# Kernel optimization log

Measured on AMD Instinct MI355X. Metric: run time of the kernel, lower is better.

The kernel has to match this reference:

```python
import jax, jax.numpy as jnp
import numpy as np

B, N, E, C, H = 2, 50000, 800000, 128, 512  # batch, nodes, edges, feat, 4*feat


def setup_inputs() -> dict:
    key = jax.random.key(0)
    ks = jax.random.split(key, 11)
    s_in = 1.0 / np.sqrt(C)
    s_h = 1.0 / np.sqrt(H)
    return {
        "graph_sig": jax.random.normal(ks[0], (B, N, C), dtype=jnp.float32),
        "edge_index": jax.random.randint(ks[1], (2, E), 0, N, dtype=jnp.int64),
        "W1_0": jax.random.normal(ks[2], (C, H), dtype=jnp.float32) * s_in,
        "b1_0": jnp.zeros((H,), dtype=jnp.float32),
        "W2_0": jax.random.normal(ks[3], (H, C), dtype=jnp.float32) * s_h,
        "b2_0": jnp.zeros((C,), dtype=jnp.float32),
        "W1_1": jax.random.normal(ks[4], (C, H), dtype=jnp.float32) * s_in,
        "b1_1": jnp.zeros((H,), dtype=jnp.float32),
        "W2_1": jax.random.normal(ks[5], (H, C), dtype=jnp.float32) * s_h,
        "b2_1": jnp.zeros((C,), dtype=jnp.float32),
    }


def gin_layer(x, src, dst, W1, b1, W2, b2):
    # GINConv with eps=0: h_i = MLP((1+eps)*x_i + sum_{j->i} x_j)
    # gather source features along edges, scatter-add into destinations
    agg = jnp.zeros_like(x).at[:, dst, :].add(x[:, src, :])  # (B, N, C)
    h = agg + x
    h = jax.nn.relu(jnp.einsum('bnc,ch->bnh', h, W1) + b1)
    return jnp.einsum('bnh,hc->bnc', h, W2) + b2


def reference(graph_sig, edge_index, W1_0, b1_0, W2_0, b2_0, W1_1, b1_1, W2_1, b2_1):
    src, dst = edge_index[0], edge_index[1]
    x = gin_layer(graph_sig, src, dst, W1_0, b1_0, W2_0, b2_0)
    x = gin_layer(x, src, dst, W1_1, b1_1, W2_1, b2_1)
    return x
```

## Files before the change

kernel.cpp:

```cpp
#include <hip/hip_runtime.h>

#define CDIM 128
#define HDIM 512
#define NB 2
#define NNODES 50000
#define NEDGES 800000
#define ROWS (NB * NNODES)

typedef _Float16 half8 __attribute__((ext_vector_type(8)));
typedef _Float16 half4 __attribute__((ext_vector_type(4)));
typedef float f32x4 __attribute__((ext_vector_type(4)));

__device__ __forceinline__ f32x4 mfma_f16(half8 a, half8 b, f32x4 c) {
  return __builtin_amdgcn_mfma_f32_16x16x32_f16(a, b, c, 0, 0, 0);
}

#define GLOAD_LDS16(g, l)                                                      \
  __builtin_amdgcn_global_load_lds(                                            \
      (const __attribute__((address_space(1))) void*)(g),                      \
      (__attribute__((address_space(3))) void*)(l), 16, 0, 0)

__global__ void hist_k(const int* __restrict__ ei, int* __restrict__ counts) {
  int e = blockIdx.x * 256 + threadIdx.x;
  if (e < NEDGES) atomicAdd(&counts[ei[NEDGES + e]], 1);
}

#define SC_BLOCKS 13

__global__ __launch_bounds__(256) void scan1_k(const int* __restrict__ counts,
                                               int* __restrict__ bsum) {
  __shared__ int ws[4];
  int i0 = blockIdx.x * 4096 + threadIdx.x * 16;
  int s = 0;
#pragma unroll
  for (int k = 0; k < 16; ++k) {
    int i = i0 + k;
    s += (i < NNODES) ? counts[i] : 0;
  }
#pragma unroll
  for (int off = 1; off < 64; off <<= 1) s += __shfl_down(s, off);
  if ((threadIdx.x & 63) == 0) ws[threadIdx.x >> 6] = s;
  __syncthreads();
  if (threadIdx.x == 0) bsum[blockIdx.x] = ws[0] + ws[1] + ws[2] + ws[3];
}

__global__ void scan2_k(const int* __restrict__ bsum, int* __restrict__ bbase,
                        int* __restrict__ offsets) {
  int run = 0;
  for (int b = 0; b < SC_BLOCKS; ++b) {
    bbase[b] = run;
    run += bsum[b];
  }
  offsets[NNODES] = run;
}

__global__ __launch_bounds__(256) void scan3_k(const int* __restrict__ counts,
                                               const int* __restrict__ bbase,
                                               int* __restrict__ offsets,
                                               int* __restrict__ cursor) {
  __shared__ int sm[256];
  int i0 = blockIdx.x * 4096 + threadIdx.x * 16;
  int v[16];
  int tsum = 0;
#pragma unroll
  for (int k = 0; k < 16; ++k) {
    int i = i0 + k;
    v[k] = (i < NNODES) ? counts[i] : 0;
    tsum += v[k];
  }
  sm[threadIdx.x] = tsum;
  __syncthreads();
  for (int off = 1; off < 256; off <<= 1) {
    int t = (threadIdx.x >= off) ? sm[threadIdx.x - off] : 0;
    __syncthreads();
    sm[threadIdx.x] += t;
    __syncthreads();
  }
  int run = bbase[blockIdx.x] + sm[threadIdx.x] - tsum;
#pragma unroll
  for (int k = 0; k < 16; ++k) {
    int i = i0 + k;
    if (i < NNODES) {
      offsets[i] = run;
      cursor[i] = run;
    }
    run += v[k];
  }
}

__global__ void fill_k(const int* __restrict__ ei, int* __restrict__ cursor,
                       int* __restrict__ col) {
  int e = blockIdx.x * 256 + threadIdx.x;
  if (e < NEDGES) {
    int d = ei[NEDGES + e];
    int p = atomicAdd(&cursor[d], 1);
    col[p] = ei[e];
  }
}

__global__ void cvt16i_k(const float* __restrict__ s, _Float16* __restrict__ d) {
  const int PB = NNODES * CDIM;
  int i = blockIdx.x * 256 + threadIdx.x;
  int str = gridDim.x * 256;
  for (; i < ROWS * (CDIM / 8); i += str) {
    size_t flat = (size_t)i * 8;
    int b = (int)(flat / PB);
    size_t r = flat - (size_t)b * PB;
    int n = (int)(r >> 7);
    int c0 = (int)(r & 127);
    float4 f0 = *(const float4*)(s + flat);
    float4 f1 = *(const float4*)(s + flat + 4);
    half8 o;
    o[0] = (_Float16)f0.x; o[1] = (_Float16)f0.y;
    o[2] = (_Float16)f0.z; o[3] = (_Float16)f0.w;
    o[4] = (_Float16)f1.x; o[5] = (_Float16)f1.y;
    o[6] = (_Float16)f1.z; o[7] = (_Float16)f1.w;
    *(half8*)(d + ((size_t)n * 2 + b) * CDIM + c0) = o;
  }
}

__global__ __launch_bounds__(256) void aggi_k(const _Float16* __restrict__ x,
                                              const int* __restrict__ offs,
                                              const int* __restrict__ col,
                                              _Float16* __restrict__ h) {
  int node = blockIdx.x * 4 + (threadIdx.x >> 6);
  int lane = threadIdx.x & 63;
  if (node >= NNODES) return;
  const half4* xp = (const half4*)x;
  half4 self = xp[(size_t)node * 64 + lane];
  float a0 = (float)self[0], a1 = (float)self[1], a2 = (float)self[2], a3 = (float)self[3];
  float c0 = 0.f, c1 = 0.f, c2 = 0.f, c3 = 0.f;
  int e = offs[node], e1 = offs[node + 1];
  for (; e + 7 < e1; e += 8) {
    int s0 = col[e], s1 = col[e + 1], s2 = col[e + 2], s3 = col[e + 3];
    int s4 = col[e + 4], s5 = col[e + 5], s6 = col[e + 6], s7 = col[e + 7];
    half4 v0 = xp[(size_t)s0 * 64 + lane];
    half4 v1 = xp[(size_t)s1 * 64 + lane];
    half4 v2 = xp[(size_t)s2 * 64 + lane];
    half4 v3 = xp[(size_t)s3 * 64 + lane];
    half4 v4 = xp[(size_t)s4 * 64 + lane];
    half4 v5 = xp[(size_t)s5 * 64 + lane];
    half4 v6 = xp[(size_t)s6 * 64 + lane];
    half4 v7 = xp[(size_t)s7 * 64 + lane];
    a0 += (float)v0[0] + (float)v1[0] + (float)v2[0] + (float)v3[0];
    a1 += (float)v0[1] + (float)v1[1] + (float)v2[1] + (float)v3[1];
    a2 += (float)v0[2] + (float)v1[2] + (float)v2[2] + (float)v3[2];
    a3 += (float)v0[3] + (float)v1[3] + (float)v2[3] + (float)v3[3];
    c0 += (float)v4[0] + (float)v5[0] + (float)v6[0] + (float)v7[0];
    c1 += (float)v4[1] + (float)v5[1] + (float)v6[1] + (float)v7[1];
    c2 += (float)v4[2] + (float)v5[2] + (float)v6[2] + (float)v7[2];
    c3 += (float)v4[3] + (float)v5[3] + (float)v6[3] + (float)v7[3];
  }
  for (; e + 1 < e1; e += 2) {
    int s0 = col[e], s1 = col[e + 1];
    half4 v0 = xp[(size_t)s0 * 64 + lane];
    half4 v1 = xp[(size_t)s1 * 64 + lane];
    a0 += (float)v0[0]; a1 += (float)v0[1];
    a2 += (float)v0[2]; a3 += (float)v0[3];
    c0 += (float)v1[0]; c1 += (float)v1[1];
    c2 += (float)v1[2]; c3 += (float)v1[3];
  }
  if (e < e1) {
    int s0 = col[e];
    half4 v0 = xp[(size_t)s0 * 64 + lane];
    a0 += (float)v0[0]; a1 += (float)v0[1];
    a2 += (float)v0[2]; a3 += (float)v0[3];
  }
  half4 r;
  r[0] = (_Float16)(a0 + c0);
  r[1] = (_Float16)(a1 + c1);
  r[2] = (_Float16)(a2 + c2);
  r[3] = (_Float16)(a3 + c3);
  ((half4*)h)[(size_t)node * 64 + lane] = r;
}

__global__ void pack_mlp(const float* __restrict__ W1, const float* __restrict__ W2,
                         _Float16* __restrict__ dst) {
  int tid = blockIdx.x * 256 + threadIdx.x;
  if (tid >= 16384) return;
  int l = tid & 63;
  int g = (tid >> 6) & 7;
  int c = (tid >> 9) & 15;
  int isW2 = tid >> 13;
  int lg = l >> 4, l15 = l & 15;
  _Float16* o;
  if (!isW2) {
    int jt = g >> 2, ks = g & 3;
    int k0 = ks * 32 + lg * 8;
    int n = c * 32 + jt * 16 + l15;
    o = dst + (size_t)c * 8192 + g * 512 + l * 8;
#pragma unroll
    for (int i = 0; i < 8; ++i) o[i] = (_Float16)W1[(size_t)(k0 + i) * HDIM + n];
  } else {
    int k0 = c * 32 + lg * 8;
    int n = g * 16 + l15;
    o = dst + (size_t)c * 8192 + 4096 + g * 512 + l * 8;
#pragma unroll
    for (int i = 0; i < 8; ++i) o[i] = (_Float16)W2[(size_t)(k0 + i) * CDIM + n];
  }
}

template <typename OT, bool REMAP>
__global__ __launch_bounds__(256, 4) void mlp_v3(
    const _Float16* __restrict__ hin, const _Float16* __restrict__ wpk,
    const float* __restrict__ b1, const float* __restrict__ b2,
    OT* __restrict__ out) {
  __shared__ alignas(16) _Float16 wbuf[2][8192];
  __shared__ alignas(16) _Float16 tbuf[4][32 * 32];

  const int tidx = threadIdx.x;
  const int lane = tidx & 63;
  const int wid = tidx >> 6;
  const int l15 = lane & 15, lg = lane >> 4;
  const long long r0 = (long long)blockIdx.x * 128 + wid * 32;

  half8 A[2][4];
#pragma unroll
  for (int rt = 0; rt < 2; ++rt) {
    long long row = r0 + rt * 16 + l15;
    if (row >= ROWS) row = ROWS - 1;
    const _Float16* hp = hin + row * CDIM + lg * 8;
#pragma unroll
    for (int ks = 0; ks < 4; ++ks) A[rt][ks] = *(const half8*)(hp + ks * 32);
  }

  {
    const _Float16* src = wpk;
#pragma unroll
    for (int q = 0; q < 4; ++q) {
      int s = wid * 4 + q;
      GLOAD_LDS16(src + s * 512 + lane * 8, &wbuf[0][s * 512]);
    }
  }
  __syncthreads();

  f32x4 acc[2][8];
#pragma unroll
  for (int rt = 0; rt < 2; ++rt)
#pragma unroll
    for (int ct = 0; ct < 8; ++ct) acc[rt][ct] = (f32x4){0.f, 0.f, 0.f, 0.f};

  _Float16* tw = &tbuf[wid][0];

  for (int c = 0; c < 16; ++c) {
    const int cur = c & 1;
    if (c + 1 < 16) {
      const _Float16* src = wpk + (size_t)(c + 1) * 8192;
#pragma unroll
      for (int q = 0; q < 4; ++q) {
        int s = wid * 4 + q;
        GLOAD_LDS16(src + s * 512 + lane * 8, &wbuf[cur ^ 1][s * 512]);
      }
    }
    const _Float16* w1c = &wbuf[cur][0];
    const _Float16* w2c = &wbuf[cur][4096];

#pragma unroll
    for (int jt = 0; jt < 2; ++jt) {
      f32x4 t0 = (f32x4){0.f, 0.f, 0.f, 0.f};
      f32x4 t1 = (f32x4){0.f, 0.f, 0.f, 0.f};
#pragma unroll
      for (int ks = 0; ks < 4; ++ks) {
        half8 b = *(const half8*)(w1c + (jt * 4 + ks) * 512 + lane * 8);
        t0 = mfma_f16(A[0][ks], b, t0);
        t1 = mfma_f16(A[1][ks], b, t1);
      }
      float bb = b1[c * 32 + jt * 16 + l15];
      int j = jt * 16 + l15;
#pragma unroll
      for (int r = 0; r < 4; ++r) {
        int n0 = lg * 4 + r;
        tw[n0 * 32 + (j ^ (((n0 >> 2) & 3) << 3))] = (_Float16)fmaxf(t0[r] + bb, 0.f);
        int n1 = 16 + lg * 4 + r;
        tw[n1 * 32 + (j ^ (((n1 >> 2) & 3) << 3))] = (_Float16)fmaxf(t1[r] + bb, 0.f);
      }
    }

    half8 ta0, ta1;
    {
      int n = l15;
      ta0 = *(const half8*)(tw + n * 32 + ((lg * 8) ^ (((n >> 2) & 3) << 3)));
      n = 16 + l15;
      ta1 = *(const half8*)(tw + n * 32 + ((lg * 8) ^ (((n >> 2) & 3) << 3)));
    }
#pragma unroll
    for (int ct = 0; ct < 8; ++ct) {
      half8 b = *(const half8*)(w2c + ct * 512 + lane * 8);
      acc[0][ct] = mfma_f16(ta0, b, acc[0][ct]);
      acc[1][ct] = mfma_f16(ta1, b, acc[1][ct]);
    }
    __syncthreads();
  }

#pragma unroll
  for (int ct = 0; ct < 8; ++ct) {
    float b2v = b2[ct * 16 + l15];
#pragma unroll
    for (int rt = 0; rt < 2; ++rt) {
#pragma unroll
      for (int r = 0; r < 4; ++r) {
        long long g = r0 + rt * 16 + lg * 4 + r;
        if (g < ROWS) {
          size_t off;
          if (REMAP) {
            off = (size_t)(g & 1) * NNODES * CDIM + (size_t)(g >> 1) * CDIM + ct * 16 + l15;
          } else {
            off = (size_t)g * CDIM + ct * 16 + l15;
          }
          out[off] = (OT)(acc[rt][ct][r] + b2v);
        }
      }
    }
  }
}

extern "C" void kernel_launch(void* const* d_in, const int* in_sizes, int n_in,
                              void* d_out, int out_size, void* d_ws, size_t ws_size,
                              hipStream_t stream) {
  const float* x0 = (const float*)d_in[0];
  const int* ei = (const int*)d_in[1];
  const float* W1_0 = (const float*)d_in[2];
  const float* b1_0 = (const float*)d_in[3];
  const float* W2_0 = (const float*)d_in[4];
  const float* b2_0 = (const float*)d_in[5];
  const float* W1_1 = (const float*)d_in[6];
  const float* b1_1 = (const float*)d_in[7];
  const float* W2_1 = (const float*)d_in[8];
  const float* b2_1 = (const float*)d_in[9];
  float* out = (float*)d_out;

  _Float16* xh = (_Float16*)d_ws;
  _Float16* hh = xh + (size_t)ROWS * CDIM;
  _Float16* wpk0 = hh + (size_t)ROWS * CDIM;
  _Float16* wpk1 = wpk0 + 131072;
  int* counts = (int*)(wpk1 + 131072);
  int* offsets = counts + NNODES;
  int* cursor = offsets + NNODES + 1;
  int* col = cursor + NNODES;
  int* bsum = col + NEDGES;
  int* bbase = bsum + 16;

  const int eBlocks = (NEDGES + 255) / 256;
  const int aggBlocks = (NNODES + 3) / 4;
  const int mlpBlocks = (ROWS + 127) / 128;

  hipMemsetAsync(counts, 0, NNODES * sizeof(int), stream);
  hist_k<<<eBlocks, 256, 0, stream>>>(ei, counts);
  scan1_k<<<SC_BLOCKS, 256, 0, stream>>>(counts, bsum);
  scan2_k<<<1, 1, 0, stream>>>(bsum, bbase, offsets);
  scan3_k<<<SC_BLOCKS, 256, 0, stream>>>(counts, bbase, offsets, cursor);
  fill_k<<<eBlocks, 256, 0, stream>>>(ei, cursor, col);

  pack_mlp<<<64, 256, 0, stream>>>(W1_0, W2_0, wpk0);
  pack_mlp<<<64, 256, 0, stream>>>(W1_1, W2_1, wpk1);

  cvt16i_k<<<2048, 256, 0, stream>>>(x0, xh);

  aggi_k<<<aggBlocks, 256, 0, stream>>>(xh, offsets, col, hh);
  mlp_v3<_Float16, false><<<mlpBlocks, 256, 0, stream>>>(hh, wpk0, b1_0, b2_0, xh);
  aggi_k<<<aggBlocks, 256, 0, stream>>>(xh, offsets, col, hh);
  mlp_v3<float, true><<<mlpBlocks, 256, 0, stream>>>(hh, wpk1, b1_1, b2_1, out);
}
```

Baseline: 338.4 us.

## Fuse neighbor aggregation into the MLP kernel via shared-memory tile

Merges the CSR gather-sum aggregation and the two-layer MLP into one kernel per GIN layer. Each wave aggregates 16 nodes (32 interleaved batch rows) into an LDS tile, then loads its MFMA A operands from that tile. This removes the global write and re-read of the aggregated features and two kernel launches. In exchange, LDS use per block rises, the launch bound drops from 4 to 2 blocks per SM, and the gather unroll shrinks from 8 to 4, which may reduce memory-level parallelism during the latency-bound gather.

```diff
diff --git a/kernel.cpp b/kernel.cpp
--- a/kernel.cpp
+++ b/kernel.cpp
@@ -119,61 +119,6 @@
   }
 }
 
-__global__ __launch_bounds__(256) void aggi_k(const _Float16* __restrict__ x,
-                                              const int* __restrict__ offs,
-                                              const int* __restrict__ col,
-                                              _Float16* __restrict__ h) {
-  int node = blockIdx.x * 4 + (threadIdx.x >> 6);
-  int lane = threadIdx.x & 63;
-  if (node >= NNODES) return;
-  const half4* xp = (const half4*)x;
-  half4 self = xp[(size_t)node * 64 + lane];
-  float a0 = (float)self[0], a1 = (float)self[1], a2 = (float)self[2], a3 = (float)self[3];
-  float c0 = 0.f, c1 = 0.f, c2 = 0.f, c3 = 0.f;
-  int e = offs[node], e1 = offs[node + 1];
-  for (; e + 7 < e1; e += 8) {
-    int s0 = col[e], s1 = col[e + 1], s2 = col[e + 2], s3 = col[e + 3];
-    int s4 = col[e + 4], s5 = col[e + 5], s6 = col[e + 6], s7 = col[e + 7];
-    half4 v0 = xp[(size_t)s0 * 64 + lane];
-    half4 v1 = xp[(size_t)s1 * 64 + lane];
-    half4 v2 = xp[(size_t)s2 * 64 + lane];
-    half4 v3 = xp[(size_t)s3 * 64 + lane];
-    half4 v4 = xp[(size_t)s4 * 64 + lane];
-    half4 v5 = xp[(size_t)s5 * 64 + lane];
-    half4 v6 = xp[(size_t)s6 * 64 + lane];
-    half4 v7 = xp[(size_t)s7 * 64 + lane];
-    a0 += (float)v0[0] + (float)v1[0] + (float)v2[0] + (float)v3[0];
-    a1 += (float)v0[1] + (float)v1[1] + (float)v2[1] + (float)v3[1];
-    a2 += (float)v0[2] + (float)v1[2] + (float)v2[2] + (float)v3[2];
-    a3 += (float)v0[3] + (float)v1[3] + (float)v2[3] + (float)v3[3];
-    c0 += (float)v4[0] + (float)v5[0] + (float)v6[0] + (float)v7[0];
-    c1 += (float)v4[1] + (float)v5[1] + (float)v6[1] + (float)v7[1];
-    c2 += (float)v4[2] + (float)v5[2] + (float)v6[2] + (float)v7[2];
-    c3 += (float)v4[3] + (float)v5[3] + (float)v6[3] + (float)v7[3];
-  }
-  for (; e + 1 < e1; e += 2) {
-    int s0 = col[e], s1 = col[e + 1];
-    half4 v0 = xp[(size_t)s0 * 64 + lane];
-    half4 v1 = xp[(size_t)s1 * 64 + lane];
-    a0 += (float)v0[0]; a1 += (float)v0[1];
-    a2 += (float)v0[2]; a3 += (float)v0[3];
-    c0 += (float)v1[0]; c1 += (float)v1[1];
-    c2 += (float)v1[2]; c3 += (float)v1[3];
-  }
-  if (e < e1) {
-    int s0 = col[e];
-    half4 v0 = xp[(size_t)s0 * 64 + lane];
-    a0 += (float)v0[0]; a1 += (float)v0[1];
-    a2 += (float)v0[2]; a3 += (float)v0[3];
-  }
-  half4 r;
-  r[0] = (_Float16)(a0 + c0);
-  r[1] = (_Float16)(a1 + c1);
-  r[2] = (_Float16)(a2 + c2);
-  r[3] = (_Float16)(a3 + c3);
-  ((half4*)h)[(size_t)node * 64 + lane] = r;
-}
-
 __global__ void pack_mlp(const float* __restrict__ W1, const float* __restrict__ W2,
                          _Float16* __restrict__ dst) {
   int tid = blockIdx.x * 256 + threadIdx.x;
@@ -201,10 +146,12 @@
 }
 
 template <typename OT, bool REMAP>
-__global__ __launch_bounds__(256, 4) void mlp_v3(
-    const _Float16* __restrict__ hin, const _Float16* __restrict__ wpk,
+__global__ __launch_bounds__(256, 2) void fused_k(
+    const _Float16* __restrict__ x, const int* __restrict__ offs,
+    const int* __restrict__ col, const _Float16* __restrict__ wpk,
     const float* __restrict__ b1, const float* __restrict__ b2,
     OT* __restrict__ out) {
+  __shared__ alignas(16) _Float16 htile[4][16 * 256];
   __shared__ alignas(16) _Float16 wbuf[2][8192];
   __shared__ alignas(16) _Float16 tbuf[4][32 * 32];
 
@@ -213,16 +160,7 @@
   const int wid = tidx >> 6;
   const int l15 = lane & 15, lg = lane >> 4;
   const long long r0 = (long long)blockIdx.x * 128 + wid * 32;
-
-  half8 A[2][4];
-#pragma unroll
-  for (int rt = 0; rt < 2; ++rt) {
-    long long row = r0 + rt * 16 + l15;
-    if (row >= ROWS) row = ROWS - 1;
-    const _Float16* hp = hin + row * CDIM + lg * 8;
-#pragma unroll
-    for (int ks = 0; ks < 4; ++ks) A[rt][ks] = *(const half8*)(hp + ks * 32);
-  }
+  const int nb = blockIdx.x * 64 + wid * 16;
 
   {
     const _Float16* src = wpk;
@@ -232,6 +170,57 @@
       GLOAD_LDS16(src + s * 512 + lane * 8, &wbuf[0][s * 512]);
     }
   }
+
+  const half4* xp = (const half4*)x;
+  _Float16* hw = &htile[wid][0];
+  for (int i = 0; i < 16; ++i) {
+    int node = nb + i;
+    half4 r = (half4){0, 0, 0, 0};
+    if (node < NNODES) {
+      half4 self = xp[(size_t)node * 64 + lane];
+      float a0 = (float)self[0], a1 = (float)self[1];
+      float a2 = (float)self[2], a3 = (float)self[3];
+      float c0 = 0.f, c1 = 0.f, c2 = 0.f, c3 = 0.f;
+      int e = offs[node], e1 = offs[node + 1];
+      for (; e + 3 < e1; e += 4) {
+        int s0 = col[e], s1 = col[e + 1], s2 = col[e + 2], s3 = col[e + 3];
+        half4 v0 = xp[(size_t)s0 * 64 + lane];
+        half4 v1 = xp[(size_t)s1 * 64 + lane];
+        half4 v2 = xp[(size_t)s2 * 64 + lane];
+        half4 v3 = xp[(size_t)s3 * 64 + lane];
+        a0 += (float)v0[0] + (float)v1[0];
+        a1 += (float)v0[1] + (float)v1[1];
+        a2 += (float)v0[2] + (float)v1[2];
+        a3 += (float)v0[3] + (float)v1[3];
+        c0 += (float)v2[0] + (float)v3[0];
+        c1 += (float)v2[1] + (float)v3[1];
+        c2 += (float)v2[2] + (float)v3[2];
+        c3 += (float)v2[3] + (float)v3[3];
+      }
+      for (; e < e1; ++e) {
+        half4 v0 = xp[(size_t)col[e] * 64 + lane];
+        a0 += (float)v0[0];
+        a1 += (float)v0[1];
+        a2 += (float)v0[2];
+        a3 += (float)v0[3];
+      }
+      r[0] = (_Float16)(a0 + c0);
+      r[1] = (_Float16)(a1 + c1);
+      r[2] = (_Float16)(a2 + c2);
+      r[3] = (_Float16)(a3 + c3);
+    }
+    *(half4*)&hw[i * 256 + lane * 4] = r;
+  }
+
+  half8 A[2][4];
+#pragma unroll
+  for (int rt = 0; rt < 2; ++rt) {
+    int rl = rt * 16 + l15;
+    const _Float16* hp = hw + (rl >> 1) * 256 + (rl & 1) * 128 + lg * 8;
+#pragma unroll
+    for (int ks = 0; ks < 4; ++ks) A[rt][ks] = *(const half8*)(hp + ks * 32);
+  }
+
   __syncthreads();
 
   f32x4 acc[2][8];
@@ -341,8 +330,7 @@
   int* bbase = bsum + 16;
 
   const int eBlocks = (NEDGES + 255) / 256;
-  const int aggBlocks = (NNODES + 3) / 4;
-  const int mlpBlocks = (ROWS + 127) / 128;
+  const int fusedBlocks = (NNODES + 63) / 64;
 
   hipMemsetAsync(counts, 0, NNODES * sizeof(int), stream);
   hist_k<<<eBlocks, 256, 0, stream>>>(ei, counts);
@@ -356,8 +344,8 @@
 
   cvt16i_k<<<2048, 256, 0, stream>>>(x0, xh);
 
-  aggi_k<<<aggBlocks, 256, 0, stream>>>(xh, offsets, col, hh);
-  mlp_v3<_Float16, false><<<mlpBlocks, 256, 0, stream>>>(hh, wpk0, b1_0, b2_0, xh);
-  aggi_k<<<aggBlocks, 256, 0, stream>>>(xh, offsets, col, hh);
-  mlp_v3<float, true><<<mlpBlocks, 256, 0, stream>>>(hh, wpk1, b1_1, b2_1, out);
-}
+  fused_k<_Float16, false><<<fusedBlocks, 256, 0, stream>>>(
+      xh, offsets, col, wpk0, b1_0, b2_0, hh);
+  fused_k<float, true><<<fusedBlocks, 256, 0, stream>>>(
+      hh, offsets, col, wpk1, b1_1, b2_1, out);
+}
```

Measured after the change: 503.7 us. +48.8%, slower.
